# Performance work log

Hardware: AMD Instinct MI355X
Metric: run time of the kernel (lower is better)

## Reference

```python
import jax, jax.numpy as jnp
import numpy as np
from jax import lax

SAMPLING_FRACTION = 0.5
BIG = 1e8  # initial 'infinite' distance, matches torch's 1e8


def _farthest_point_sample(points, init_idx, n_sample):
    """points: (B,N,C) float; init_idx: (B,) int. Returns (B, n_sample) int32 indices."""
    B, N, C = points.shape
    batch = jnp.arange(B)

    def step(carry, _):
        distances, farthest = carry            # (B,N), (B,)
        centroid = points[batch, farthest]     # (B,C)
        d = jnp.sum((points - centroid[:, None, :]) ** 2, axis=-1)  # (B,N) squared euclid
        distances = jnp.minimum(distances, d)
        new_farthest = jnp.argmax(distances, axis=-1)
        return (distances, new_farthest), farthest  # record index BEFORE update (matches torch)

    init = (jnp.full((B, N), BIG, dtype=points.dtype), init_idx.astype(jnp.int32))
    _, centroids = lax.scan(step, init, None, length=n_sample)
    return centroids.T  # (B, n_sample)


def _index_points(x, idx):
    # x: (B, N, ...) ; idx: (B, M) -> (B, M, ...)
    return jnp.take_along_axis(x, idx.reshape(idx.shape + (1,) * (x.ndim - 2)), axis=1) if x.ndim > 2 else jnp.take_along_axis(x, idx, axis=1)


def setup_inputs() -> dict:
    key = jax.random.key(0)
    k1, k2, k3 = jax.random.split(key, 3)
    B, N, C, D = 16, 8192, 3, 256
    coords = jax.random.normal(k1, (B, N, C), dtype=jnp.float32)
    values = jax.random.normal(k2, (B, N, D), dtype=jnp.float32)
    mask = jnp.ones((B, N), dtype=jnp.float32)
    init_idx = jax.random.randint(k3, (B,), 0, N)
    return {"coords": coords, "values": values, "mask": mask, "init_idx": init_idx}


def reference(coords, values, mask, init_idx):
    B, N, C = coords.shape
    n_sample = int(round(N * SAMPLING_FRACTION))
    idx = _farthest_point_sample(coords, init_idx, n_sample)  # (B, n_sample)
    query_coords = _index_points(coords, idx)  # (B, M, C)
    query_values = _index_points(values, idx)  # (B, M, D)
    query_mask = _index_points(mask, idx)      # (B, M)
    return (query_coords, query_values, query_mask)
```

## Files before the change

### kernel.cpp

```cpp
#include <hip/hip_runtime.h>

typedef unsigned long long u64;
typedef float v2f __attribute__((ext_vector_type(2)));

#define FPS_N   8192
#define FPS_T   256
#define FPS_W   (FPS_T / 64)
#define FPS_PPT (FPS_N / FPS_T)
#define FPS_PR  (FPS_PPT / 2)

__device__ __forceinline__ v2f pk_add(v2f a, v2f b) {
    v2f r; asm("v_pk_add_f32 %0, %1, %2" : "=v"(r) : "v"(a), "v"(b)); return r;
}
__device__ __forceinline__ v2f pk_mul(v2f a, v2f b) {
    v2f r; asm("v_pk_mul_f32 %0, %1, %2" : "=v"(r) : "v"(a), "v"(b)); return r;
}
__device__ __forceinline__ v2f pk_fma(v2f a, v2f b, v2f c) {
    v2f r; asm("v_pk_fma_f32 %0, %1, %2, %3" : "=v"(r) : "v"(a), "v"(b), "v"(c)); return r;
}

template<int CTRL>
__device__ __forceinline__ float dpp_max_step(float x) {
    int s = __builtin_amdgcn_update_dpp(0, __float_as_int(x), CTRL, 0xf, 0xf, true);
    return fmaxf(x, __int_as_float(s));
}
__device__ __forceinline__ float wave_max_nn(float x) {
    x = dpp_max_step<0x111>(x);
    x = dpp_max_step<0x112>(x);
    x = dpp_max_step<0x114>(x);
    x = dpp_max_step<0x118>(x);
    x = dpp_max_step<0x142>(x);
    x = dpp_max_step<0x143>(x);
    return __int_as_float(__builtin_amdgcn_readlane(__float_as_int(x), 63));
}
__device__ __forceinline__ float readlane_f(float x, int l) {
    return __int_as_float(__builtin_amdgcn_readlane(__float_as_int(x), l));
}

__global__ __launch_bounds__(FPS_T, 1) void fps_kernel(
    const float* __restrict__ coords,
    const int*   __restrict__ init_idx,
    int*         __restrict__ out_idx,
    int M)
{
    __shared__ float sx[FPS_N], sy[FPS_N], sz[FPS_N];
    __shared__ u64 mbox[2][FPS_W];

    const int b    = blockIdx.x;
    const int tid  = threadIdx.x;
    const int lane = tid & 63;
    const int wv   = tid >> 6;
    const float* cb = coords + (size_t)b * FPS_N * 3;

    if (tid < 2 * FPS_W) ((u64*)mbox)[tid] = 0ull;

    float f[96];
    const float4* cb4 = reinterpret_cast<const float4*>(cb);
    #pragma unroll
    for (int i = 0; i < 24; ++i) {
        float4 v = cb4[tid * 24 + i];
        f[i*4+0] = v.x; f[i*4+1] = v.y; f[i*4+2] = v.z; f[i*4+3] = v.w;
    }

    v2f px[FPS_PR], py[FPS_PR], pz[FPS_PR], dist[FPS_PR];
    const int base = tid * FPS_PPT;
    #pragma unroll
    for (int k = 0; k < FPS_PPT; ++k) {
        sx[base+k] = f[3*k+0]; sy[base+k] = f[3*k+1]; sz[base+k] = f[3*k+2];
    }
    #pragma unroll
    for (int j = 0; j < FPS_PR; ++j) {
        px[j] = v2f{f[6*j+0], f[6*j+3]};
        py[j] = v2f{f[6*j+1], f[6*j+4]};
        pz[j] = v2f{f[6*j+2], f[6*j+5]};
        dist[j] = v2f{1e8f, 1e8f};
    }
    __syncthreads();

    int far = init_idx[b];
    float cx = sx[far], cy = sy[far], cz = sz[far];

    int buf[16];
    #pragma unroll
    for (int i = 0; i < 16; ++i) buf[i] = 0;

    for (int so = 0; so < M; so += 16) {
        const int owner = so >> 4;
        #pragma unroll
        for (int si = 0; si < 16; ++si) {
            const int s = so + si;
            if (tid == owner) buf[si] = far;

            const v2f ncx = v2f{-cx, -cx};
            const v2f ncy = v2f{-cy, -cy};
            const v2f ncz = v2f{-cz, -cz};
            float m = 0.0f;
            #pragma unroll
            for (int j = 0; j < FPS_PR; ++j) {
                v2f dx2 = pk_add(px[j], ncx);
                v2f dy2 = pk_add(py[j], ncy);
                v2f dz2 = pk_add(pz[j], ncz);
                v2f d2  = pk_fma(dz2, dz2, pk_fma(dy2, dy2, pk_mul(dx2, dx2)));
                v2f nd;
                nd.x = fminf(dist[j].x, d2.x);
                nd.y = fminf(dist[j].y, d2.y);
                dist[j] = nd;
                m = fmaxf(m, fmaxf(nd.x, nd.y));
            }
            int myidx = base;
            #pragma unroll
            for (int j = FPS_PR - 1; j >= 0; --j) {
                myidx = (dist[j].y == m) ? base + 2*j + 1 : myidx;
                myidx = (dist[j].x == m) ? base + 2*j     : myidx;
            }

            float wm = wave_max_nn(m);
            u64 ball = __ballot(m == wm);
            int fl   = (int)__builtin_ctzll(ball);
            int widx = __builtin_amdgcn_readlane(myidx, fl);

            const int par = s & 1;
            if (lane == 0) {
                u64 pk = ((u64)(unsigned)__float_as_uint(wm) << 32)
                       | ((u64)(unsigned)widx << 13)
                       | (u64)(unsigned)(s + 1);
                __hip_atomic_store(&mbox[par][wv], pk,
                                   __ATOMIC_RELAXED, __HIP_MEMORY_SCOPE_WORKGROUP);
            }

            const unsigned tag = (unsigned)(s + 1);
            u64 v;
            do {
                v = __hip_atomic_load(&mbox[par][lane & (FPS_W - 1)],
                                      __ATOMIC_RELAXED, __HIP_MEMORY_SCOPE_WORKGROUP);
            } while (!__all((unsigned)(v & 0x1FFFull) == tag));

            float cand = __int_as_float((int)(v >> 32));
            int   cidx = (int)((v >> 13) & 0x1FFF);
            float fx = sx[cidx], fy = sy[cidx], fz = sz[cidx];
            float g = cand;
            g = dpp_max_step<0x111>(g);
            g = dpp_max_step<0x112>(g);
            float gm = readlane_f(g, 3);
            u64 b2 = __ballot(cand == gm);
            int l2 = (int)__builtin_ctzll(b2);
            far = __builtin_amdgcn_readlane(cidx, l2);
            cx  = readlane_f(fx, l2);
            cy  = readlane_f(fy, l2);
            cz  = readlane_f(fz, l2);
        }
    }

    int4* ob = reinterpret_cast<int4*>(out_idx + (size_t)b * M + tid * 16);
    ob[0] = int4{buf[0],  buf[1],  buf[2],  buf[3]};
    ob[1] = int4{buf[4],  buf[5],  buf[6],  buf[7]};
    ob[2] = int4{buf[8],  buf[9],  buf[10], buf[11]};
    ob[3] = int4{buf[12], buf[13], buf[14], buf[15]};
}

__global__ void gather_kernel(
    const float* __restrict__ coords,
    const float* __restrict__ values,
    const float* __restrict__ mask,
    const int*   __restrict__ idx,
    float* __restrict__ out_coords,
    float* __restrict__ out_values,
    float* __restrict__ out_mask,
    int N, int M, int D)
{
    const int bm = blockIdx.x;
    const int b  = bm / M;
    const int m  = bm - b * M;
    const int j  = idx[bm];
    const int l  = threadIdx.x;

    const float4* src = reinterpret_cast<const float4*>(values + ((size_t)b * N + j) * D);
    float4*       dst = reinterpret_cast<float4*>(out_values + ((size_t)b * M + m) * D);
    dst[l] = src[l];

    if (l < 3) {
        out_coords[((size_t)b * M + m) * 3 + l] = coords[((size_t)b * N + j) * 3 + l];
    } else if (l == 3) {
        out_mask[(size_t)b * M + m] = mask[(size_t)b * N + j];
    }
}

extern "C" void kernel_launch(void* const* d_in, const int* in_sizes, int n_in,
                              void* d_out, int out_size, void* d_ws, size_t ws_size,
                              hipStream_t stream)
{
    const float* coords   = (const float*)d_in[0];
    const float* values   = (const float*)d_in[1];
    const float* mask     = (const float*)d_in[2];
    const int*   init_idx = (const int*)d_in[3];

    const int B = in_sizes[3];
    const int N = in_sizes[2] / B;
    const int D = in_sizes[1] / (B * N);
    const int M = N / 2;

    float* out_coords = (float*)d_out;
    float* out_values = out_coords + (size_t)B * M * 3;
    float* out_mask   = out_values + (size_t)B * M * D;

    int* idx = (int*)d_ws;

    fps_kernel<<<B, FPS_T, 0, stream>>>(coords, init_idx, idx, M);
    gather_kernel<<<B * M, D / 4, 0, stream>>>(coords, values, mask, idx,
                                               out_coords, out_values, out_mask,
                                               N, M, D);
}
```

Measured before the change: 3.507 ms.

## Replace tagged mailbox spin-wait with barrier and cheapen per-thread argmax

Swaps the per-iteration cross-wave exchange from packed 64-bit atomic mailbox writes plus a spin loop for split float/int shared arrays followed by __syncthreads. It also reworks the per-thread argmax: it keeps a per-pair max, finds the winning pair index, then picks x or y, which cuts the compare/select chain. The barrier replaces polling with a hardware sync. Double buffering by parity keeps the single barrier safe, but a full workgroup barrier on every one of the thousands of serial steps may cost more or less than the spin.

Result: slower. 3.593 ms (+2.5%).

```diff
diff --git a/kernel.cpp b/kernel.cpp
--- a/kernel.cpp
+++ b/kernel.cpp
@@ -44,15 +44,14 @@
     int M)
 {
     __shared__ float sx[FPS_N], sy[FPS_N], sz[FPS_N];
-    __shared__ u64 mbox[2][FPS_W];
+    __shared__ float swd[2][FPS_W];
+    __shared__ int   swi[2][FPS_W];
 
     const int b    = blockIdx.x;
     const int tid  = threadIdx.x;
     const int lane = tid & 63;
     const int wv   = tid >> 6;
     const float* cb = coords + (size_t)b * FPS_N * 3;
-
-    if (tid < 2 * FPS_W) ((u64*)mbox)[tid] = 0ull;
 
     float f[96];
     const float4* cb4 = reinterpret_cast<const float4*>(cb);
@@ -94,6 +93,7 @@
             const v2f ncx = v2f{-cx, -cx};
             const v2f ncy = v2f{-cy, -cy};
             const v2f ncz = v2f{-cz, -cz};
+            float pm[FPS_PR];
             float m = 0.0f;
             #pragma unroll
             for (int j = 0; j < FPS_PR; ++j) {
@@ -105,14 +105,19 @@
                 nd.x = fminf(dist[j].x, d2.x);
                 nd.y = fminf(dist[j].y, d2.y);
                 dist[j] = nd;
-                m = fmaxf(m, fmaxf(nd.x, nd.y));
+                pm[j] = fmaxf(nd.x, nd.y);
+                m = fmaxf(m, pm[j]);
             }
-            int myidx = base;
+            int jw = 0;
             #pragma unroll
-            for (int j = FPS_PR - 1; j >= 0; --j) {
-                myidx = (dist[j].y == m) ? base + 2*j + 1 : myidx;
-                myidx = (dist[j].x == m) ? base + 2*j     : myidx;
-            }
+            for (int j = FPS_PR - 1; j >= 0; --j)
+                jw = (pm[j] == m) ? j : jw;
+            int myidx = base + 2 * jw;
+            float dxh = pm[0];
+            #pragma unroll
+            for (int j = 0; j < FPS_PR; ++j)
+                dxh = (j == jw) ? dist[j].x : dxh;
+            myidx += (dxh == m) ? 0 : 1;
 
             float wm = wave_max_nn(m);
             u64 ball = __ballot(m == wm);
@@ -121,22 +126,13 @@
 
             const int par = s & 1;
             if (lane == 0) {
-                u64 pk = ((u64)(unsigned)__float_as_uint(wm) << 32)
-                       | ((u64)(unsigned)widx << 13)
-                       | (u64)(unsigned)(s + 1);
-                __hip_atomic_store(&mbox[par][wv], pk,
-                                   __ATOMIC_RELAXED, __HIP_MEMORY_SCOPE_WORKGROUP);
+                swd[par][wv] = wm;
+                swi[par][wv] = widx;
             }
-
-            const unsigned tag = (unsigned)(s + 1);
-            u64 v;
-            do {
-                v = __hip_atomic_load(&mbox[par][lane & (FPS_W - 1)],
-                                      __ATOMIC_RELAXED, __HIP_MEMORY_SCOPE_WORKGROUP);
-            } while (!__all((unsigned)(v & 0x1FFFull) == tag));
-
-            float cand = __int_as_float((int)(v >> 32));
-            int   cidx = (int)((v >> 13) & 0x1FFF);
+            __syncthreads();
+
+            float cand = swd[par][lane & (FPS_W - 1)];
+            int   cidx = swi[par][lane & (FPS_W - 1)];
             float fx = sx[cidx], fy = sy[cidx], fz = sz[cidx];
             float g = cand;
             g = dpp_max_step<0x111>(g);
```

## Process two batches per FPS block to overlap their reduction latencies

Applied to the files above, without the earlier changes.

Each FPS workgroup now handles two batch elements at once. The two distance updates and reductions are interleaved so that one batch's cross-wave mailbox handoff latency is hidden behind the other's ALU work. The centroid coordinates are now fetched from global memory instead of an LDS copy, which removes the shared coordinate arrays. The cost is double register pressure (about 128 extra VGPRs for points and distances), half as many blocks, and a dependent global load on the serial critical path each step.

Result: slower. 6.812 ms (+94.3%).

```diff
diff --git a/kernel.cpp b/kernel.cpp
--- a/kernel.cpp
+++ b/kernel.cpp
@@ -43,119 +43,186 @@
     int*         __restrict__ out_idx,
     int M)
 {
-    __shared__ float sx[FPS_N], sy[FPS_N], sz[FPS_N];
-    __shared__ u64 mbox[2][FPS_W];
-
-    const int b    = blockIdx.x;
+    __shared__ u64 mbox[2][2][FPS_W];
+
+    const int blk  = blockIdx.x;
+    const int bA   = blk * 2, bB = blk * 2 + 1;
     const int tid  = threadIdx.x;
     const int lane = tid & 63;
     const int wv   = tid >> 6;
-    const float* cb = coords + (size_t)b * FPS_N * 3;
-
-    if (tid < 2 * FPS_W) ((u64*)mbox)[tid] = 0ull;
-
-    float f[96];
-    const float4* cb4 = reinterpret_cast<const float4*>(cb);
+    const float* cbA = coords + (size_t)bA * FPS_N * 3;
+    const float* cbB = coords + (size_t)bB * FPS_N * 3;
+    const int base = tid * FPS_PPT;
+
+    if (tid < 16) ((u64*)mbox)[tid] = 0ull;
+
+    v2f pxA[FPS_PR], pyA[FPS_PR], pzA[FPS_PR], dAv[FPS_PR];
+    {
+        float f[96];
+        const float4* c4 = reinterpret_cast<const float4*>(cbA);
+        #pragma unroll
+        for (int i = 0; i < 24; ++i) {
+            float4 v = c4[tid * 24 + i];
+            f[i*4+0] = v.x; f[i*4+1] = v.y; f[i*4+2] = v.z; f[i*4+3] = v.w;
+        }
+        #pragma unroll
+        for (int j = 0; j < FPS_PR; ++j) {
+            pxA[j] = v2f{f[6*j+0], f[6*j+3]};
+            pyA[j] = v2f{f[6*j+1], f[6*j+4]};
+            pzA[j] = v2f{f[6*j+2], f[6*j+5]};
+            dAv[j] = v2f{1e8f, 1e8f};
+        }
+    }
+    v2f pxB[FPS_PR], pyB[FPS_PR], pzB[FPS_PR], dBv[FPS_PR];
+    {
+        float f[96];
+        const float4* c4 = reinterpret_cast<const float4*>(cbB);
+        #pragma unroll
+        for (int i = 0; i < 24; ++i) {
+            float4 v = c4[tid * 24 + i];
+            f[i*4+0] = v.x; f[i*4+1] = v.y; f[i*4+2] = v.z; f[i*4+3] = v.w;
+        }
+        #pragma unroll
+        for (int j = 0; j < FPS_PR; ++j) {
+            pxB[j] = v2f{f[6*j+0], f[6*j+3]};
+            pyB[j] = v2f{f[6*j+1], f[6*j+4]};
+            pzB[j] = v2f{f[6*j+2], f[6*j+5]};
+            dBv[j] = v2f{1e8f, 1e8f};
+        }
+    }
+    __syncthreads();
+
+    int farA = init_idx[bA], farB = init_idx[bB];
+    float cxA = cbA[farA*3+0], cyA = cbA[farA*3+1], czA = cbA[farA*3+2];
+    float cxB = cbB[farB*3+0], cyB = cbB[farB*3+1], czB = cbB[farB*3+2];
+
+    int bufA[16], bufB[16];
     #pragma unroll
-    for (int i = 0; i < 24; ++i) {
-        float4 v = cb4[tid * 24 + i];
-        f[i*4+0] = v.x; f[i*4+1] = v.y; f[i*4+2] = v.z; f[i*4+3] = v.w;
-    }
-
-    v2f px[FPS_PR], py[FPS_PR], pz[FPS_PR], dist[FPS_PR];
-    const int base = tid * FPS_PPT;
-    #pragma unroll
-    for (int k = 0; k < FPS_PPT; ++k) {
-        sx[base+k] = f[3*k+0]; sy[base+k] = f[3*k+1]; sz[base+k] = f[3*k+2];
-    }
-    #pragma unroll
-    for (int j = 0; j < FPS_PR; ++j) {
-        px[j] = v2f{f[6*j+0], f[6*j+3]};
-        py[j] = v2f{f[6*j+1], f[6*j+4]};
-        pz[j] = v2f{f[6*j+2], f[6*j+5]};
-        dist[j] = v2f{1e8f, 1e8f};
-    }
-    __syncthreads();
-
-    int far = init_idx[b];
-    float cx = sx[far], cy = sy[far], cz = sz[far];
-
-    int buf[16];
-    #pragma unroll
-    for (int i = 0; i < 16; ++i) buf[i] = 0;
+    for (int i = 0; i < 16; ++i) { bufA[i] = 0; bufB[i] = 0; }
 
     for (int so = 0; so < M; so += 16) {
         const int owner = so >> 4;
         #pragma unroll
         for (int si = 0; si < 16; ++si) {
             const int s = so + si;
-            if (tid == owner) buf[si] = far;
-
-            const v2f ncx = v2f{-cx, -cx};
-            const v2f ncy = v2f{-cy, -cy};
-            const v2f ncz = v2f{-cz, -cz};
-            float m = 0.0f;
+            if (tid == owner) { bufA[si] = farA; bufB[si] = farB; }
+
+            const v2f ncxA = v2f{-cxA, -cxA};
+            const v2f ncyA = v2f{-cyA, -cyA};
+            const v2f nczA = v2f{-czA, -czA};
+            float mA = 0.0f;
             #pragma unroll
             for (int j = 0; j < FPS_PR; ++j) {
-                v2f dx2 = pk_add(px[j], ncx);
-                v2f dy2 = pk_add(py[j], ncy);
-                v2f dz2 = pk_add(pz[j], ncz);
+                v2f dx2 = pk_add(pxA[j], ncxA);
+                v2f dy2 = pk_add(pyA[j], ncyA);
+                v2f dz2 = pk_add(pzA[j], nczA);
                 v2f d2  = pk_fma(dz2, dz2, pk_fma(dy2, dy2, pk_mul(dx2, dx2)));
                 v2f nd;
-                nd.x = fminf(dist[j].x, d2.x);
-                nd.y = fminf(dist[j].y, d2.y);
-                dist[j] = nd;
-                m = fmaxf(m, fmaxf(nd.x, nd.y));
-            }
-            int myidx = base;
+                nd.x = fminf(dAv[j].x, d2.x);
+                nd.y = fminf(dAv[j].y, d2.y);
+                dAv[j] = nd;
+                mA = fmaxf(mA, fmaxf(nd.x, nd.y));
+            }
+            const v2f ncxB = v2f{-cxB, -cxB};
+            const v2f ncyB = v2f{-cyB, -cyB};
+            const v2f nczB = v2f{-czB, -czB};
+            float mB = 0.0f;
+            #pragma unroll
+            for (int j = 0; j < FPS_PR; ++j) {
+                v2f dx2 = pk_add(pxB[j], ncxB);
+                v2f dy2 = pk_add(pyB[j], ncyB);
+                v2f dz2 = pk_add(pzB[j], nczB);
+                v2f d2  = pk_fma(dz2, dz2, pk_fma(dy2, dy2, pk_mul(dx2, dx2)));
+                v2f nd;
+                nd.x = fminf(dBv[j].x, d2.x);
+                nd.y = fminf(dBv[j].y, d2.y);
+                dBv[j] = nd;
+                mB = fmaxf(mB, fmaxf(nd.x, nd.y));
+            }
+
+            int myidxA = base;
             #pragma unroll
             for (int j = FPS_PR - 1; j >= 0; --j) {
-                myidx = (dist[j].y == m) ? base + 2*j + 1 : myidx;
-                myidx = (dist[j].x == m) ? base + 2*j     : myidx;
-            }
-
-            float wm = wave_max_nn(m);
-            u64 ball = __ballot(m == wm);
-            int fl   = (int)__builtin_ctzll(ball);
-            int widx = __builtin_amdgcn_readlane(myidx, fl);
+                myidxA = (dAv[j].y == mA) ? base + 2*j + 1 : myidxA;
+                myidxA = (dAv[j].x == mA) ? base + 2*j     : myidxA;
+            }
+            int myidxB = base;
+            #pragma unroll
+            for (int j = FPS_PR - 1; j >= 0; --j) {
+                myidxB = (dBv[j].y == mB) ? base + 2*j + 1 : myidxB;
+                myidxB = (dBv[j].x == mB) ? base + 2*j     : myidxB;
+            }
+
+            float wmA = wave_max_nn(mA);
+            float wmB = wave_max_nn(mB);
+            u64 ballA = __ballot(mA == wmA);
+            u64 ballB = __ballot(mB == wmB);
+            int flA = (int)__builtin_ctzll(ballA);
+            int flB = (int)__builtin_ctzll(ballB);
+            int widxA = __builtin_amdgcn_readlane(myidxA, flA);
+            int widxB = __builtin_amdgcn_readlane(myidxB, flB);
 
             const int par = s & 1;
+            const unsigned tag = (unsigned)(s + 1);
             if (lane == 0) {
-                u64 pk = ((u64)(unsigned)__float_as_uint(wm) << 32)
-                       | ((u64)(unsigned)widx << 13)
-                       | (u64)(unsigned)(s + 1);
-                __hip_atomic_store(&mbox[par][wv], pk,
+                u64 pkA = ((u64)(unsigned)__float_as_uint(wmA) << 32)
+                        | ((u64)(unsigned)widxA << 13) | (u64)tag;
+                u64 pkB = ((u64)(unsigned)__float_as_uint(wmB) << 32)
+                        | ((u64)(unsigned)widxB << 13) | (u64)tag;
+                __hip_atomic_store(&mbox[0][par][wv], pkA,
                                    __ATOMIC_RELAXED, __HIP_MEMORY_SCOPE_WORKGROUP);
-            }
-
-            const unsigned tag = (unsigned)(s + 1);
-            u64 v;
+                __hip_atomic_store(&mbox[1][par][wv], pkB,
+                                   __ATOMIC_RELAXED, __HIP_MEMORY_SCOPE_WORKGROUP);
+            }
+
+            const int sl = lane & (FPS_W - 1);
+            u64 va, vb;
             do {
-                v = __hip_atomic_load(&mbox[par][lane & (FPS_W - 1)],
-                                      __ATOMIC_RELAXED, __HIP_MEMORY_SCOPE_WORKGROUP);
-            } while (!__all((unsigned)(v & 0x1FFFull) == tag));
-
-            float cand = __int_as_float((int)(v >> 32));
-            int   cidx = (int)((v >> 13) & 0x1FFF);
-            float fx = sx[cidx], fy = sy[cidx], fz = sz[cidx];
-            float g = cand;
-            g = dpp_max_step<0x111>(g);
-            g = dpp_max_step<0x112>(g);
-            float gm = readlane_f(g, 3);
-            u64 b2 = __ballot(cand == gm);
-            int l2 = (int)__builtin_ctzll(b2);
-            far = __builtin_amdgcn_readlane(cidx, l2);
-            cx  = readlane_f(fx, l2);
-            cy  = readlane_f(fy, l2);
-            cz  = readlane_f(fz, l2);
-        }
-    }
-
-    int4* ob = reinterpret_cast<int4*>(out_idx + (size_t)b * M + tid * 16);
-    ob[0] = int4{buf[0],  buf[1],  buf[2],  buf[3]};
-    ob[1] = int4{buf[4],  buf[5],  buf[6],  buf[7]};
-    ob[2] = int4{buf[8],  buf[9],  buf[10], buf[11]};
-    ob[3] = int4{buf[12], buf[13], buf[14], buf[15]};
+                va = __hip_atomic_load(&mbox[0][par][sl],
+                                       __ATOMIC_RELAXED, __HIP_MEMORY_SCOPE_WORKGROUP);
+                vb = __hip_atomic_load(&mbox[1][par][sl],
+                                       __ATOMIC_RELAXED, __HIP_MEMORY_SCOPE_WORKGROUP);
+            } while (!__all(((unsigned)(va & 0x1FFFull) == tag) &
+                            ((unsigned)(vb & 0x1FFFull) == tag)));
+
+            {
+                float cand = __int_as_float((int)(va >> 32));
+                int   cidx = (int)((va >> 13) & 0x1FFF);
+                float g = cand;
+                g = dpp_max_step<0x111>(g);
+                g = dpp_max_step<0x112>(g);
+                float gm = readlane_f(g, 3);
+                u64 b2 = __ballot(cand == gm);
+                int l2 = (int)__builtin_ctzll(b2);
+                farA = __builtin_amdgcn_readlane(cidx, l2);
+            }
+            cxA = cbA[farA*3+0]; cyA = cbA[farA*3+1]; czA = cbA[farA*3+2];
+
+            {
+                float cand = __int_as_float((int)(vb >> 32));
+                int   cidx = (int)((vb >> 13) & 0x1FFF);
+                float g = cand;
+                g = dpp_max_step<0x111>(g);
+                g = dpp_max_step<0x112>(g);
+                float gm = readlane_f(g, 3);
+                u64 b2 = __ballot(cand == gm);
+                int l2 = (int)__builtin_ctzll(b2);
+                farB = __builtin_amdgcn_readlane(cidx, l2);
+            }
+            cxB = cbB[farB*3+0]; cyB = cbB[farB*3+1]; czB = cbB[farB*3+2];
+        }
+    }
+
+    int4* obA = reinterpret_cast<int4*>(out_idx + (size_t)bA * M + tid * 16);
+    obA[0] = int4{bufA[0],  bufA[1],  bufA[2],  bufA[3]};
+    obA[1] = int4{bufA[4],  bufA[5],  bufA[6],  bufA[7]};
+    obA[2] = int4{bufA[8],  bufA[9],  bufA[10], bufA[11]};
+    obA[3] = int4{bufA[12], bufA[13], bufA[14], bufA[15]};
+    int4* obB = reinterpret_cast<int4*>(out_idx + (size_t)bB * M + tid * 16);
+    obB[0] = int4{bufB[0],  bufB[1],  bufB[2],  bufB[3]};
+    obB[1] = int4{bufB[4],  bufB[5],  bufB[6],  bufB[7]};
+    obB[2] = int4{bufB[8],  bufB[9],  bufB[10], bufB[11]};
+    obB[3] = int4{bufB[12], bufB[13], bufB[14], bufB[15]};
 }
 
 __global__ void gather_kernel(
@@ -205,7 +272,7 @@
 
     int* idx = (int*)d_ws;
 
-    fps_kernel<<<B, FPS_T, 0, stream>>>(coords, init_idx, idx, M);
+    fps_kernel<<<B / 2, FPS_T, 0, stream>>>(coords, init_idx, idx, M);
     gather_kernel<<<B * M, D / 4, 0, stream>>>(coords, values, mask, idx,
                                                out_coords, out_values, out_mask,
                                                N, M, D);
```

## Pack two batches per FPS block and drop LDS coordinate copy

Applied to the files above, without the earlier changes.

Each FPS workgroup now handles two batch elements with 512 threads: two independent 256-thread groups, each with its own mailbox slots. The shared-memory coordinate arrays are removed, and the next centroid is read directly from global memory (served by cache) after each step. The per-thread argmax is also fused into the distance loop instead of a second equality scan. This halves the block count, which may help or hurt SM/CU-level latency hiding. It also adds a dependent global load on the serial critical path of every iteration.

Measured after the change: 5.692 ms. 62.3% more time.

```diff
diff --git a/kernel.cpp b/kernel.cpp
--- a/kernel.cpp
+++ b/kernel.cpp
@@ -4,9 +4,10 @@
 typedef float v2f __attribute__((ext_vector_type(2)));
 
 #define FPS_N   8192
-#define FPS_T   256
-#define FPS_W   (FPS_T / 64)
-#define FPS_PPT (FPS_N / FPS_T)
+#define FPS_T   512
+#define FPS_GW  4
+#define FPS_GT  256
+#define FPS_PPT (FPS_N / FPS_GT)
 #define FPS_PR  (FPS_PPT / 2)
 
 __device__ __forceinline__ v2f pk_add(v2f a, v2f b) {
@@ -37,37 +38,34 @@
     return __int_as_float(__builtin_amdgcn_readlane(__float_as_int(x), l));
 }
 
-__global__ __launch_bounds__(FPS_T, 1) void fps_kernel(
+__global__ __launch_bounds__(FPS_T) void fps_kernel(
     const float* __restrict__ coords,
     const int*   __restrict__ init_idx,
     int*         __restrict__ out_idx,
     int M)
 {
-    __shared__ float sx[FPS_N], sy[FPS_N], sz[FPS_N];
-    __shared__ u64 mbox[2][FPS_W];
-
-    const int b    = blockIdx.x;
-    const int tid  = threadIdx.x;
-    const int lane = tid & 63;
-    const int wv   = tid >> 6;
+    __shared__ u64 mbox[2][2][FPS_GW];
+
+    const int tid   = threadIdx.x;
+    const int grp   = tid >> 8;
+    const int tg    = tid & (FPS_GT - 1);
+    const int lane  = tid & 63;
+    const int wvg   = (tid >> 6) & (FPS_GW - 1);
+    const int b     = blockIdx.x * 2 + grp;
     const float* cb = coords + (size_t)b * FPS_N * 3;
-
-    if (tid < 2 * FPS_W) ((u64*)mbox)[tid] = 0ull;
+    const int base  = tg * FPS_PPT;
+
+    if (tid < 16) ((u64*)mbox)[tid] = 0ull;
 
     float f[96];
     const float4* cb4 = reinterpret_cast<const float4*>(cb);
     #pragma unroll
     for (int i = 0; i < 24; ++i) {
-        float4 v = cb4[tid * 24 + i];
+        float4 v = cb4[tg * 24 + i];
         f[i*4+0] = v.x; f[i*4+1] = v.y; f[i*4+2] = v.z; f[i*4+3] = v.w;
     }
 
     v2f px[FPS_PR], py[FPS_PR], pz[FPS_PR], dist[FPS_PR];
-    const int base = tid * FPS_PPT;
-    #pragma unroll
-    for (int k = 0; k < FPS_PPT; ++k) {
-        sx[base+k] = f[3*k+0]; sy[base+k] = f[3*k+1]; sz[base+k] = f[3*k+2];
-    }
     #pragma unroll
     for (int j = 0; j < FPS_PR; ++j) {
         px[j] = v2f{f[6*j+0], f[6*j+3]};
@@ -78,7 +76,7 @@
     __syncthreads();
 
     int far = init_idx[b];
-    float cx = sx[far], cy = sy[far], cz = sz[far];
+    float cx = cb[far*3+0], cy = cb[far*3+1], cz = cb[far*3+2];
 
     int buf[16];
     #pragma unroll
@@ -89,12 +87,13 @@
         #pragma unroll
         for (int si = 0; si < 16; ++si) {
             const int s = so + si;
-            if (tid == owner) buf[si] = far;
+            if (tg == owner) buf[si] = far;
 
             const v2f ncx = v2f{-cx, -cx};
             const v2f ncy = v2f{-cy, -cy};
             const v2f ncz = v2f{-cz, -cz};
             float m = 0.0f;
+            int   mi = base;
             #pragma unroll
             for (int j = 0; j < FPS_PR; ++j) {
                 v2f dx2 = pk_add(px[j], ncx);
@@ -105,39 +104,35 @@
                 nd.x = fminf(dist[j].x, d2.x);
                 nd.y = fminf(dist[j].y, d2.y);
                 dist[j] = nd;
-                m = fmaxf(m, fmaxf(nd.x, nd.y));
-            }
-            int myidx = base;
-            #pragma unroll
-            for (int j = FPS_PR - 1; j >= 0; --j) {
-                myidx = (dist[j].y == m) ? base + 2*j + 1 : myidx;
-                myidx = (dist[j].x == m) ? base + 2*j     : myidx;
+                float pmax = fmaxf(nd.x, nd.y);
+                int   ex   = (nd.x >= nd.y) ? base + 2*j : base + 2*j + 1;
+                bool  upd  = pmax > m;
+                m  = upd ? pmax : m;
+                mi = upd ? ex   : mi;
             }
 
             float wm = wave_max_nn(m);
             u64 ball = __ballot(m == wm);
             int fl   = (int)__builtin_ctzll(ball);
-            int widx = __builtin_amdgcn_readlane(myidx, fl);
+            int widx = __builtin_amdgcn_readlane(mi, fl);
 
             const int par = s & 1;
+            const unsigned tag = (unsigned)(s + 1);
             if (lane == 0) {
                 u64 pk = ((u64)(unsigned)__float_as_uint(wm) << 32)
-                       | ((u64)(unsigned)widx << 13)
-                       | (u64)(unsigned)(s + 1);
-                __hip_atomic_store(&mbox[par][wv], pk,
+                       | ((u64)(unsigned)widx << 13) | (u64)tag;
+                __hip_atomic_store(&mbox[grp][par][wvg], pk,
                                    __ATOMIC_RELAXED, __HIP_MEMORY_SCOPE_WORKGROUP);
             }
 
-            const unsigned tag = (unsigned)(s + 1);
             u64 v;
             do {
-                v = __hip_atomic_load(&mbox[par][lane & (FPS_W - 1)],
+                v = __hip_atomic_load(&mbox[grp][par][lane & (FPS_GW - 1)],
                                       __ATOMIC_RELAXED, __HIP_MEMORY_SCOPE_WORKGROUP);
             } while (!__all((unsigned)(v & 0x1FFFull) == tag));
 
             float cand = __int_as_float((int)(v >> 32));
             int   cidx = (int)((v >> 13) & 0x1FFF);
-            float fx = sx[cidx], fy = sy[cidx], fz = sz[cidx];
             float g = cand;
             g = dpp_max_step<0x111>(g);
             g = dpp_max_step<0x112>(g);
@@ -145,13 +140,11 @@
             u64 b2 = __ballot(cand == gm);
             int l2 = (int)__builtin_ctzll(b2);
             far = __builtin_amdgcn_readlane(cidx, l2);
-            cx  = readlane_f(fx, l2);
-            cy  = readlane_f(fy, l2);
-            cz  = readlane_f(fz, l2);
+            cx = cb[far*3+0]; cy = cb[far*3+1]; cz = cb[far*3+2];
         }
     }
 
-    int4* ob = reinterpret_cast<int4*>(out_idx + (size_t)b * M + tid * 16);
+    int4* ob = reinterpret_cast<int4*>(out_idx + (size_t)b * M + tg * 16);
     ob[0] = int4{buf[0],  buf[1],  buf[2],  buf[3]};
     ob[1] = int4{buf[4],  buf[5],  buf[6],  buf[7]};
     ob[2] = int4{buf[8],  buf[9],  buf[10], buf[11]};
@@ -205,7 +198,7 @@
 
     int* idx = (int*)d_ws;
 
-    fps_kernel<<<B, FPS_T, 0, stream>>>(coords, init_idx, idx, M);
+    fps_kernel<<<B / 2, FPS_T, 0, stream>>>(coords, init_idx, idx, M);
     gather_kernel<<<B * M, D / 4, 0, stream>>>(coords, values, mask, idx,
                                                out_coords, out_values, out_mask,
                                                N, M, D);
```
